# Kernel optimization log

Hardware: AMD Instinct MI355X
Metric: run time of the kernel (lower is better)

## Reference

```python
import jax, jax.numpy as jnp
import numpy as np

B, S, D, H = 4, 2048, 1024, 16
HD = D // H  # 64


def setup_inputs() -> dict:
    key = jax.random.key(0)
    ks = jax.random.split(key, 5)
    s = 1.0 / np.sqrt(D)
    return {
        "x": jax.random.normal(ks[0], (B, S, D), dtype=jnp.float32),
        "W_attn": jax.random.normal(ks[1], (D, 3 * D), dtype=jnp.float32) * s,
        "b_attn": jnp.zeros((3 * D,), dtype=jnp.float32),
        "W_proj": jax.random.normal(ks[2], (D, D), dtype=jnp.float32) * s,
        "b_proj": jnp.zeros((D,), dtype=jnp.float32),
    }


def reference(x, W_attn, b_attn, W_proj, b_proj):
    Bx, Sx, Dx = x.shape
    qkv = x @ W_attn + b_attn                      # [B,S,3D]
    q, k, v = jnp.split(qkv, 3, axis=-1)
    q = q.reshape(Bx, Sx, H, HD).transpose(0, 2, 1, 3)  # [B,H,S,hd]
    k = k.reshape(Bx, Sx, H, HD).transpose(0, 2, 1, 3)
    v = v.reshape(Bx, Sx, H, HD).transpose(0, 2, 1, 3)
    att = jnp.einsum('bhqd,bhkd->bhqk', q, k) * (HD ** -0.5)
    causal = jnp.tril(jnp.ones((Sx, Sx), dtype=bool))
    att = jnp.where(causal[None, None], att, -jnp.inf)
    att = jax.nn.softmax(att, axis=-1)
    y = jnp.einsum('bhqk,bhkd->bhqd', att, v)      # [B,H,S,hd]
    y = y.transpose(0, 2, 1, 3).reshape(Bx, Sx, Dx)
    return y @ W_proj + b_proj
```

## Files before the change

kernel.cpp:

```cpp
#include <hip/hip_runtime.h>
#include <hip/hip_bf16.h>
#include <math.h>


typedef __bf16 bf16;
typedef __bf16 bf16x8 __attribute__((ext_vector_type(8)));
typedef __bf16 bf16x4 __attribute__((ext_vector_type(4)));
typedef float f32x4 __attribute__((ext_vector_type(4)));

#define B_ 4
#define S_ 2048
#define D_ 1024
#define H_ 16
#define HD_ 64
#define QSCALE 0.1803368801f

#if __has_builtin(__builtin_amdgcn_exp2f)
#define EXP2F(x) __builtin_amdgcn_exp2f(x)
#else
#define EXP2F(x) exp2f(x)
#endif
#if __has_builtin(__builtin_amdgcn_rcpf)
#define RCPF(x) __builtin_amdgcn_rcpf(x)
#else
#define RCPF(x) (1.0f / (x))
#endif

#define GLOAD_LDS16(gptr, lptr)                                              \
    __builtin_amdgcn_global_load_lds(                                        \
        (const __attribute__((address_space(1))) void*)(uintptr_t)(gptr),    \
        (__attribute__((address_space(3))) void*)(uintptr_t)(lptr), 16, 0, 0)

template <int CTRL>
__device__ __forceinline__ float dpp_mov_f(float x) {
    int xi = __builtin_bit_cast(int, x);
    int r = __builtin_amdgcn_mov_dpp(xi, CTRL, 0xF, 0xF, true);
    return __builtin_bit_cast(float, r);
}
__device__ __forceinline__ float rowsum16(float x) {
    x += dpp_mov_f<0xB1>(x);
    x += dpp_mov_f<0x4E>(x);
    x += dpp_mov_f<0x124>(x);
    x += dpp_mov_f<0x128>(x);
    return x;
}

__global__ void k_cvt(const float* __restrict__ in, bf16* __restrict__ out, int n) {
    int i = (blockIdx.x * 256 + threadIdx.x) * 4;
    if (i >= n) return;
    float4 v = *reinterpret_cast<const float4*>(in + i);
    bf16x4 o;
    o.x = (bf16)v.x; o.y = (bf16)v.y; o.z = (bf16)v.z; o.w = (bf16)v.w;
    *reinterpret_cast<bf16x4*>(out + i) = o;
}

__global__ void k_transpose_cvt(const float* __restrict__ W, bf16* __restrict__ WT,
                                int K, int N) {
    __shared__ float t[32][33];
    int n0 = blockIdx.x * 32, k0 = blockIdx.y * 32;
    int tx = threadIdx.x & 31, ty = threadIdx.x >> 5;
#pragma unroll
    for (int j = 0; j < 32; j += 8)
        t[ty + j][tx] = W[(size_t)(k0 + ty + j) * N + n0 + tx];
    __syncthreads();
#pragma unroll
    for (int j = 0; j < 32; j += 8)
        WT[(size_t)(n0 + ty + j) * K + k0 + tx] = (bf16)t[tx][ty + j];
}

template <int MODE>
__global__ __launch_bounds__(256) void k_gemm(
    const bf16* __restrict__ A, const bf16* __restrict__ BT,
    const float* __restrict__ bias,
    void* out0, void* out1, void* out2, int M, int N, int K) {
    __shared__ __align__(16) bf16 Asm[128 * 32];
    __shared__ __align__(16) bf16 Bsm[128 * 32];
    int mb = blockIdx.y * 128, nb = blockIdx.x * 128;
    int tid = threadIdx.x;
    int w = tid >> 6, lane = tid & 63, lo = lane & 15, qu = lane >> 4;
    int wm = (w >> 1) * 64, wn = (w & 1) * 64;
    int srow_in_wave = lane >> 2;
    int schunk = lane & 3;
    f32x4 zero = {0.f, 0.f, 0.f, 0.f};
    f32x4 acc[4][4];
#pragma unroll
    for (int i = 0; i < 4; i++)
#pragma unroll
        for (int j = 0; j < 4; j++) acc[i][j] = zero;

    int fswz = (lo >> 1) & 3;

    for (int kb = 0; kb < K; kb += 32) {
        __syncthreads();
#pragma unroll
        for (int u = 0; u < 2; u++) {
            int row0 = w * 32 + u * 16;
            int row = row0 + srow_in_wave;
            int cg = schunk ^ ((row >> 1) & 3);
            GLOAD_LDS16(A + (size_t)(mb + row) * K + kb + cg * 8, &Asm[row0 * 32]);
            GLOAD_LDS16(BT + (size_t)(nb + row) * K + kb + cg * 8, &Bsm[row0 * 32]);
        }
        __syncthreads();
        bf16x8 af[4], bfr[4];
#pragma unroll
        for (int t = 0; t < 4; t++) {
            af[t]  = *reinterpret_cast<const bf16x8*>(
                &Asm[(wm + t * 16 + lo) * 32 + (qu ^ fswz) * 8]);
            bfr[t] = *reinterpret_cast<const bf16x8*>(
                &Bsm[(wn + t * 16 + lo) * 32 + (qu ^ fswz) * 8]);
        }
#pragma unroll
        for (int i = 0; i < 4; i++)
#pragma unroll
            for (int j = 0; j < 4; j++)
                acc[i][j] = __builtin_amdgcn_mfma_f32_16x16x32_bf16(af[i], bfr[j],
                                                                    acc[i][j], 0, 0, 0);
    }
#pragma unroll
    for (int i = 0; i < 4; i++) {
#pragma unroll
        for (int j = 0; j < 4; j++) {
            int col = nb + wn + j * 16 + lo;
            float bv = bias[col];
            float v4v[4];
#pragma unroll
            for (int r = 0; r < 4; r++) v4v[r] = acc[i][j][r] + bv;
            int row0 = mb + wm + i * 16 + qu * 4;
            if (MODE == 0) {
                int b = row0 >> 11, s0 = row0 & 2047;
                int which = col >> 10, rem = col & 1023;
                int h = rem >> 6, d = rem & 63;
                int bh = b * H_ + h;
                if (which == 2) {
                    bf16x4 pk;
#pragma unroll
                    for (int r = 0; r < 4; r++) pk[r] = (bf16)v4v[r];
                    *reinterpret_cast<bf16x4*>(
                        (bf16*)out2 + ((size_t)bh * HD_ + d) * S_ + s0) = pk;
                } else {
                    bf16* dst = which == 0 ? (bf16*)out0 : (bf16*)out1;
                    float sc = which == 0 ? QSCALE : 1.0f;
#pragma unroll
                    for (int r = 0; r < 4; r++)
                        dst[((size_t)bh * S_ + s0 + r) * HD_ + d] = (bf16)(v4v[r] * sc);
                }
            } else {
#pragma unroll
                for (int r = 0; r < 4; r++)
                    ((float*)out0)[(size_t)(row0 + r) * N + col] = v4v[r];
            }
        }
    }
}

__global__ __launch_bounds__(256) void k_attn(
    const bf16* __restrict__ Q, const bf16* __restrict__ K,
    const bf16* __restrict__ Vt, bf16* __restrict__ Y) {
    __shared__ __align__(16) bf16 Ks[2][64][64];
    __shared__ __align__(16) bf16 Vs[2][64][64];
    __shared__ __align__(16) bf16 Psm[4][32][72];
    int blk = blockIdx.x;
    int bh = blk & 63;
    int jb = 15 - (blk >> 6);
    int tid = threadIdx.x, w = tid >> 6, lane = tid & 63;
    int lo = lane & 15, qu = lane >> 4;
    int b = bh >> 4, h = bh & 15;
    int qbase = jb * 128 + w * 32;
    const bf16* Qb = Q + (size_t)bh * S_ * HD_;
    const bf16* Kb = K + (size_t)bh * S_ * HD_;
    const bf16* Vb = Vt + (size_t)bh * HD_ * S_;

    bf16x8 qf[2][2];
#pragma unroll
    for (int i = 0; i < 2; i++)
#pragma unroll
        for (int ks = 0; ks < 2; ks++)
            qf[i][ks] = *reinterpret_cast<const bf16x8*>(
                Qb + (size_t)(qbase + i * 16 + lo) * HD_ + ks * 32 + qu * 8);

    f32x4 zero = {0.f, 0.f, 0.f, 0.f};
    f32x4 o[2][4];
    float l_i[2][4];
#pragma unroll
    for (int i = 0; i < 2; i++)
#pragma unroll
        for (int r = 0; r < 4; r++) { o[i][r] = zero; l_i[i][r] = 0.f; }

    int nt = 2 * jb + 2;
    int r0 = w * 16;
    int lrow = lane >> 3, lch = lane & 7;
    int gch = (lch ^ lrow) * 8;

    auto stageKV = [&](int t, int buf) {
        int kb = t * 64;
#pragma unroll
        for (int s = 0; s < 2; s++) {
            int row = r0 + s * 8;
            GLOAD_LDS16(Kb + (size_t)(kb + row + lrow) * HD_ + gch,
                        &Ks[buf][row][0]);
            GLOAD_LDS16(Vb + (size_t)(row + lrow) * S_ + kb + gch,
                        &Vs[buf][row][0]);
        }
    };

    stageKV(0, 0);

    for (int t = 0; t < nt; t++) {
        int cur = t & 1;
        if (t + 1 < nt) {
            stageKV(t + 1, cur ^ 1);
            asm volatile("s_waitcnt vmcnt(4)" ::: "memory");
        } else {
            asm volatile("s_waitcnt vmcnt(0)" ::: "memory");
        }
        __builtin_amdgcn_s_barrier();
        asm volatile("" ::: "memory");
        int kb = t * 64;
        if (kb <= qbase + 31) {
            bf16x8 kf[4][2];
#pragma unroll
            for (int kc = 0; kc < 4; kc++)
#pragma unroll
                for (int ks = 0; ks < 2; ks++)
                    kf[kc][ks] = *reinterpret_cast<const bf16x8*>(
                        &Ks[cur][kc * 16 + lo][((ks * 4 + qu) ^ (lo & 7)) * 8]);
            f32x4 sc[2][4];
#pragma unroll
            for (int kc = 0; kc < 4; kc++)
#pragma unroll
                for (int i = 0; i < 2; i++) {
                    f32x4 a = __builtin_amdgcn_mfma_f32_16x16x32_bf16(
                        qf[i][0], kf[kc][0], zero, 0, 0, 0);
                    sc[i][kc] = __builtin_amdgcn_mfma_f32_16x16x32_bf16(
                        qf[i][1], kf[kc][1], a, 0, 0, 0);
                }
            bf16x8 vfr[4][2];
#pragma unroll
            for (int nc = 0; nc < 4; nc++)
#pragma unroll
                for (int ks = 0; ks < 2; ks++)
                    vfr[nc][ks] = *reinterpret_cast<const bf16x8*>(
                        &Vs[cur][nc * 16 + lo][((ks * 4 + qu) ^ (lo & 7)) * 8]);
            if (kb + 63 > qbase) {
#pragma unroll
                for (int kc = 0; kc < 4; kc++) {
                    int kj = kb + kc * 16 + lo;
#pragma unroll
                    for (int i = 0; i < 2; i++) {
                        int qi = qbase + i * 16 + qu * 4;
#pragma unroll
                        for (int r = 0; r < 4; r++)
                            sc[i][kc][r] = (kj > qi + r) ? -1e30f : sc[i][kc][r];
                    }
                }
            }
#pragma unroll
            for (int i = 0; i < 2; i++)
#pragma unroll
                for (int kc = 0; kc < 4; kc++)
#pragma unroll
                    for (int r = 0; r < 4; r++)
                        sc[i][kc][r] = EXP2F(sc[i][kc][r]);
#pragma unroll
            for (int i = 0; i < 2; i++)
#pragma unroll
                for (int r = 0; r < 4; r++) {
                    float s = (sc[i][0][r] + sc[i][1][r]) + (sc[i][2][r] + sc[i][3][r]);
                    l_i[i][r] += rowsum16(s);
                }
#pragma unroll
            for (int i = 0; i < 2; i++)
#pragma unroll
                for (int kc = 0; kc < 4; kc++)
#pragma unroll
                    for (int r = 0; r < 4; r++)
                        Psm[w][i * 16 + qu * 4 + r][kc * 16 + lo] = (bf16)sc[i][kc][r];
            asm volatile("s_waitcnt lgkmcnt(0)" ::: "memory");
            bf16x8 pa[2][2];
#pragma unroll
            for (int i = 0; i < 2; i++)
#pragma unroll
                for (int ks = 0; ks < 2; ks++)
                    pa[i][ks] = *reinterpret_cast<const bf16x8*>(
                        &Psm[w][i * 16 + lo][ks * 32 + qu * 8]);
#pragma unroll
            for (int nc = 0; nc < 4; nc++)
#pragma unroll
                for (int i = 0; i < 2; i++) {
                    o[i][nc] = __builtin_amdgcn_mfma_f32_16x16x32_bf16(
                        pa[i][0], vfr[nc][0], o[i][nc], 0, 0, 0);
                    o[i][nc] = __builtin_amdgcn_mfma_f32_16x16x32_bf16(
                        pa[i][1], vfr[nc][1], o[i][nc], 0, 0, 0);
                }
        }
        asm volatile("" ::: "memory");
        __builtin_amdgcn_s_barrier();
        asm volatile("" ::: "memory");
    }

#pragma unroll
    for (int i = 0; i < 2; i++) {
#pragma unroll
        for (int r = 0; r < 4; r++) {
            float inv = RCPF(l_i[i][r]);
            int s = qbase + i * 16 + qu * 4 + r;
#pragma unroll
            for (int nc = 0; nc < 4; nc++) {
                float v = o[i][nc][r] * inv;
                Y[((size_t)(b * S_ + s) * H_ + h) * HD_ + nc * 16 + lo] = (bf16)v;
            }
        }
    }
}

extern "C" void kernel_launch(void* const* d_in, const int* in_sizes, int n_in,
                              void* d_out, int out_size, void* d_ws, size_t ws_size,
                              hipStream_t stream) {
    const float* x      = (const float*)d_in[0];
    const float* W_attn = (const float*)d_in[1];
    const float* b_attn = (const float*)d_in[2];
    const float* W_proj = (const float*)d_in[3];
    const float* b_proj = (const float*)d_in[4];
    float* out = (float*)d_out;

    char* ws = (char*)d_ws;
    size_t off = 0;
    auto alloc = [&](size_t bytes) -> void* {
        void* p = ws + off;
        off += (bytes + 255) & ~(size_t)255;
        return p;
    };
    const size_t MD = (size_t)B_ * S_ * D_;
    bf16* xb  = (bf16*)alloc(MD * 2);
    bf16* wta = (bf16*)alloc((size_t)3 * D_ * D_ * 2);
    bf16* wtp = (bf16*)alloc((size_t)D_ * D_ * 2);
    bf16* Qb  = (bf16*)alloc(MD * 2);
    bf16* Kb  = (bf16*)alloc(MD * 2);
    bf16* Vtb = (bf16*)alloc(MD * 2);
    bf16* Ya  = (bf16*)alloc(MD * 2);

    k_cvt<<<8192, 256, 0, stream>>>(x, xb, (int)MD);
    k_transpose_cvt<<<dim3(96, 32), 256, 0, stream>>>(W_attn, wta, D_, 3 * D_);
    k_transpose_cvt<<<dim3(32, 32), 256, 0, stream>>>(W_proj, wtp, D_, D_);
    k_gemm<0><<<dim3(24, 64), 256, 0, stream>>>(xb, wta, b_attn, Qb, Kb, Vtb,
                                                B_ * S_, 3 * D_, D_);
    k_attn<<<dim3(1024), 256, 0, stream>>>(Qb, Kb, Vtb, Ya);
    k_gemm<1><<<dim3(8, 64), 256, 0, stream>>>(Ya, wtp, b_proj, out, nullptr, nullptr,
                                               B_ * S_, D_, D_);
}
```

Before: 276.1 us.

## Compute softmax row sums via MFMA against ones, add setprio, shrink P padding

Replaces the per-row DPP shuffle reductions of the softmax denominator with extra MFMA instructions that multiply the bf16 P tile by a vector of ones, accumulating the row sums in matrix-core accumulators. Wraps the QK and PV MFMA sections in s_setprio to raise wave priority during matrix work, and changes the P shared-memory row padding from 72 to 68. This moves VALU/DPP work onto the matrix cores, but the row sums are now taken from bf16-rounded P rather than fp32 values, and the new padding may change LDS bank conflicts.

```diff
diff --git a/kernel.cpp b/kernel.cpp
--- a/kernel.cpp
+++ b/kernel.cpp
@@ -30,20 +30,6 @@
     __builtin_amdgcn_global_load_lds(                                        \
         (const __attribute__((address_space(1))) void*)(uintptr_t)(gptr),    \
         (__attribute__((address_space(3))) void*)(uintptr_t)(lptr), 16, 0, 0)
-
-template <int CTRL>
-__device__ __forceinline__ float dpp_mov_f(float x) {
-    int xi = __builtin_bit_cast(int, x);
-    int r = __builtin_amdgcn_mov_dpp(xi, CTRL, 0xF, 0xF, true);
-    return __builtin_bit_cast(float, r);
-}
-__device__ __forceinline__ float rowsum16(float x) {
-    x += dpp_mov_f<0xB1>(x);
-    x += dpp_mov_f<0x4E>(x);
-    x += dpp_mov_f<0x124>(x);
-    x += dpp_mov_f<0x128>(x);
-    return x;
-}
 
 __global__ void k_cvt(const float* __restrict__ in, bf16* __restrict__ out, int n) {
     int i = (blockIdx.x * 256 + threadIdx.x) * 4;
@@ -158,7 +144,7 @@
     const bf16* __restrict__ Vt, bf16* __restrict__ Y) {
     __shared__ __align__(16) bf16 Ks[2][64][64];
     __shared__ __align__(16) bf16 Vs[2][64][64];
-    __shared__ __align__(16) bf16 Psm[4][32][72];
+    __shared__ __align__(16) bf16 Psm[4][32][68];
     int blk = blockIdx.x;
     int bh = blk & 63;
     int jb = 15 - (blk >> 6);
@@ -178,13 +164,19 @@
             qf[i][ks] = *reinterpret_cast<const bf16x8*>(
                 Qb + (size_t)(qbase + i * 16 + lo) * HD_ + ks * 32 + qu * 8);
 
+    bf16x8 onesf;
+#pragma unroll
+    for (int j = 0; j < 8; j++) onesf[j] = (bf16)1.0f;
+
     f32x4 zero = {0.f, 0.f, 0.f, 0.f};
     f32x4 o[2][4];
-    float l_i[2][4];
-#pragma unroll
-    for (int i = 0; i < 2; i++)
-#pragma unroll
-        for (int r = 0; r < 4; r++) { o[i][r] = zero; l_i[i][r] = 0.f; }
+    f32x4 lacc[2];
+#pragma unroll
+    for (int i = 0; i < 2; i++) {
+        lacc[i] = zero;
+#pragma unroll
+        for (int r = 0; r < 4; r++) o[i][r] = zero;
+    }
 
     int nt = 2 * jb + 2;
     int r0 = w * 16;
@@ -225,6 +217,7 @@
                     kf[kc][ks] = *reinterpret_cast<const bf16x8*>(
                         &Ks[cur][kc * 16 + lo][((ks * 4 + qu) ^ (lo & 7)) * 8]);
             f32x4 sc[2][4];
+            __builtin_amdgcn_s_setprio(1);
 #pragma unroll
             for (int kc = 0; kc < 4; kc++)
 #pragma unroll
@@ -234,6 +227,7 @@
                     sc[i][kc] = __builtin_amdgcn_mfma_f32_16x16x32_bf16(
                         qf[i][1], kf[kc][1], a, 0, 0, 0);
                 }
+            __builtin_amdgcn_s_setprio(0);
             bf16x8 vfr[4][2];
 #pragma unroll
             for (int nc = 0; nc < 4; nc++)
@@ -264,13 +258,6 @@
 #pragma unroll
             for (int i = 0; i < 2; i++)
 #pragma unroll
-                for (int r = 0; r < 4; r++) {
-                    float s = (sc[i][0][r] + sc[i][1][r]) + (sc[i][2][r] + sc[i][3][r]);
-                    l_i[i][r] += rowsum16(s);
-                }
-#pragma unroll
-            for (int i = 0; i < 2; i++)
-#pragma unroll
                 for (int kc = 0; kc < 4; kc++)
 #pragma unroll
                     for (int r = 0; r < 4; r++)
@@ -283,6 +270,14 @@
                 for (int ks = 0; ks < 2; ks++)
                     pa[i][ks] = *reinterpret_cast<const bf16x8*>(
                         &Psm[w][i * 16 + lo][ks * 32 + qu * 8]);
+            __builtin_amdgcn_s_setprio(1);
+#pragma unroll
+            for (int i = 0; i < 2; i++) {
+                lacc[i] = __builtin_amdgcn_mfma_f32_16x16x32_bf16(
+                    pa[i][0], onesf, lacc[i], 0, 0, 0);
+                lacc[i] = __builtin_amdgcn_mfma_f32_16x16x32_bf16(
+                    pa[i][1], onesf, lacc[i], 0, 0, 0);
+            }
 #pragma unroll
             for (int nc = 0; nc < 4; nc++)
 #pragma unroll
@@ -292,6 +287,7 @@
                     o[i][nc] = __builtin_amdgcn_mfma_f32_16x16x32_bf16(
                         pa[i][1], vfr[nc][1], o[i][nc], 0, 0, 0);
                 }
+            __builtin_amdgcn_s_setprio(0);
         }
         asm volatile("" ::: "memory");
         __builtin_amdgcn_s_barrier();
@@ -302,7 +298,7 @@
     for (int i = 0; i < 2; i++) {
 #pragma unroll
         for (int r = 0; r < 4; r++) {
-            float inv = RCPF(l_i[i][r]);
+            float inv = RCPF(lacc[i][r]);
             int s = qbase + i * 16 + qu * 4 + r;
 #pragma unroll
             for (int nc = 0; nc < 4; nc++) {
```

New measurement: 272.8 us. No clear change (-1.2%).
